# Performance work log

Measured on AMD Instinct MI355X. Metric: run time of the kernel, lower is better.

Reference implementation:

```python
import jax, jax.numpy as jnp
import numpy as np

N = 50000
E = 800000
H = 256
ED = 13
EPS = 1e-5


def silu(x):
    return x * jax.nn.sigmoid(x)


def layernorm(x, g, b):
    mu = jnp.mean(x, axis=-1, keepdims=True)
    var = jnp.var(x, axis=-1, keepdims=True)
    return (x - mu) * jax.lax.rsqrt(var + EPS) * g + b


def setup_inputs() -> dict:
    key = jax.random.key(0)
    ks = jax.random.split(key, 24)
    s = 0.02
    d = {
        "h": jax.random.normal(ks[0], (N, H), jnp.float32),
        "pos": jax.random.normal(ks[1], (N, 3), jnp.float32),
        "edge_index": jax.random.randint(ks[2], (2, E), 0, N, jnp.int32),
        "edge_attr": jax.random.normal(ks[3], (E, ED), jnp.float32),
        # edge_mlp: Linear(2H+1+ED -> 2H), SiLU, LN(2H), Linear(2H -> H), SiLU
        "W_e1": jax.random.normal(ks[4], (2 * H + 1 + ED, 2 * H), jnp.float32) * s,
        "b_e1": jnp.zeros((2 * H,), jnp.float32),
        "g_e": jnp.ones((2 * H,), jnp.float32),
        "be_ln": jnp.zeros((2 * H,), jnp.float32),
        "W_e2": jax.random.normal(ks[5], (2 * H, H), jnp.float32) * s,
        "b_e2": jnp.zeros((H,), jnp.float32),
        # node_mlp: Linear(2H -> 2H), SiLU, LN(2H), Linear(2H -> H)
        "W_n1": jax.random.normal(ks[6], (2 * H, 2 * H), jnp.float32) * s,
        "b_n1": jnp.zeros((2 * H,), jnp.float32),
        "g_n": jnp.ones((2 * H,), jnp.float32),
        "bn_ln": jnp.zeros((2 * H,), jnp.float32),
        "W_n2": jax.random.normal(ks[7], (2 * H, H), jnp.float32) * s,
        "b_n2": jnp.zeros((H,), jnp.float32),
        # outer LayerNorm(H)
        "g_o": jnp.ones((H,), jnp.float32),
        "bo_ln": jnp.zeros((H,), jnp.float32),
        # coord_mlp: Linear(H->H), SiLU, Linear(H->1, no bias, weight*0.001)
        "W_c1": jax.random.normal(ks[8], (H, H), jnp.float32) * s,
        "b_c1": jnp.zeros((H,), jnp.float32),
        "W_c2": jax.random.normal(ks[9], (H, 1), jnp.float32) * 0.001,
        # att_mlp: Linear(H->1), Sigmoid
        "W_a": jax.random.normal(ks[10], (H, 1), jnp.float32) * s,
        "b_a": jnp.zeros((1,), jnp.float32),
        # coord_feedback: Linear(1->H), SiLU, Linear(H->H)
        "W_f1": jax.random.normal(ks[11], (1, H), jnp.float32) * s,
        "b_f1": jnp.zeros((H,), jnp.float32),
        "W_f2": jax.random.normal(ks[12], (H, H), jnp.float32) * s,
        "b_f2": jnp.zeros((H,), jnp.float32),
    }
    return d


def reference(h, pos, edge_index, edge_attr,
              W_e1, b_e1, g_e, be_ln, W_e2, b_e2,
              W_n1, b_n1, g_n, bn_ln, W_n2, b_n2,
              g_o, bo_ln,
              W_c1, b_c1, W_c2,
              W_a, b_a,
              W_f1, b_f1, W_f2, b_f2):
    row, col = edge_index[0], edge_index[1]
    diff = pos[row] - pos[col]                                  # [E,3]
    dist = jnp.maximum(jnp.linalg.norm(diff, axis=-1, keepdims=True), 1e-5)
    edge_in = jnp.concatenate([h[row], h[col], dist, edge_attr], axis=-1)
    m = silu(layernorm(silu(edge_in @ W_e1 + b_e1), g_e, be_ln) @ W_e2 + b_e2)  # [E,H]
    att = jax.nn.sigmoid(m @ W_a + b_a)                         # [E,1]
    agg = jax.ops.segment_sum(m * att, row, num_segments=N)     # [N,H]
    node_in = jnp.concatenate([h, agg], axis=-1)
    h_upd = layernorm(silu(node_in @ W_n1 + b_n1), g_n, bn_ln) @ W_n2 + b_n2
    h_new = layernorm(h + h_upd, g_o, bo_ln)
    coord_w = silu(m @ W_c1 + b_c1) @ W_c2                      # [E,1]
    coord_agg = jax.ops.segment_sum(diff * coord_w, row, num_segments=N)
    pos_new = pos + coord_agg
    diff_new = pos_new[row] - pos_new[col]
    dist_new = jnp.maximum(jnp.linalg.norm(diff_new, axis=-1, keepdims=True), 1e-5)
    coord_fb = silu(dist_new @ W_f1 + b_f1) @ W_f2 + b_f2       # [E,H]
    fb_agg = jax.ops.segment_sum(coord_fb, row, num_segments=N)
    h_new = h_new + 0.1 * fb_agg
    return (h_new, pos_new)
```

## Files before the change

kernel.cpp:

```cpp
#include <hip/hip_runtime.h>


#define NN 50000
#define EE 800000

typedef unsigned short u16;
typedef float f32x4 __attribute__((ext_vector_type(4)));
typedef short bf16x8 __attribute__((ext_vector_type(8)));
typedef unsigned uint4v __attribute__((ext_vector_type(4)));

__device__ __forceinline__ u16 f2bf(float f) {
  unsigned u = __float_as_uint(f);
  u = (u + 0x7FFFu + ((u >> 16) & 1u)) >> 16;
  return (u16)u;
}
__device__ __forceinline__ float bf2f(u16 s) {
  return __uint_as_float(((unsigned)s) << 16);
}
__device__ __forceinline__ float bflo(unsigned u) { return __uint_as_float(u << 16); }
__device__ __forceinline__ float bfhi(unsigned u) { return __uint_as_float(u & 0xFFFF0000u); }
__device__ __forceinline__ float silu_f(float x) {
  return x * __builtin_amdgcn_rcpf(1.f + exp2f(x * -1.44269504f));
}

__device__ __forceinline__ void gload16(const void* g, void* l) {
  __builtin_amdgcn_global_load_lds(
      (const __attribute__((address_space(1))) void*)g,
      (__attribute__((address_space(3))) void*)l, 16, 0, 0);
}

__global__ __launch_bounds__(256, 2) void edge_fused(
    const u16* __restrict__ P1, const u16* __restrict__ P2,
    const float* __restrict__ dist, const float* __restrict__ eattr,
    const float* __restrict__ Wt, const float* __restrict__ ge,
    const float* __restrict__ beln, const float* __restrict__ be2,
    const float* __restrict__ bc1, const float* __restrict__ Wa,
    const float* __restrict__ ba, const float* __restrict__ Wc2,
    const u16* __restrict__ We2s, const u16* __restrict__ Wc1s,
    const int* __restrict__ rowp, const int* __restrict__ colp,
    const int* __restrict__ perm, const int* __restrict__ meta, int cidx,
    u16* __restrict__ mBuf, float* __restrict__ att, float* __restrict__ cwv) {
  const int M = meta[2 * cidx + 1];
  const int eb = meta[2 * cidx];
  const int m0 = blockIdx.x * 64;
  if (m0 >= M) return;
  __shared__ __align__(16) u16 At[64][512];
  __shared__ __align__(16) u16 Bs[4][64][32];
  const int tid = threadIdx.x, w = tid >> 6, lane = tid & 63;
  const int l15 = lane & 15, kq = lane >> 4;
  const int ch0 = lane * 8;
  const int sr = lane >> 2, sl = lane & 3;

  {
    float wreg[8][15], gg[8], bb[8];
#pragma unroll
    for (int i = 0; i < 8; i++) {
#pragma unroll
      for (int j = 0; j < 15; j++) wreg[i][j] = Wt[(ch0 + i) * 16 + j];
      gg[i] = ge[ch0 + i]; bb[i] = beln[ch0 + i];
    }
#pragma unroll 2
    for (int rr = 0; rr < 16; rr++) {
      int row = w * 16 + rr;
      int le = m0 + row; if (le > M - 1) le = M - 1;
      int e = perm[eb + le];
      int r = rowp[e], c = colp[e];
      float dd = dist[e];
      float fa[13];
#pragma unroll
      for (int j = 0; j < 13; j++) fa[j] = eattr[(size_t)e * 13 + j];
      uint4v u1 = *(const uint4v*)&P1[(size_t)r * 512 + ch0];
      uint4v u2 = *(const uint4v*)&P2[(size_t)c * 512 + ch0];
      float sv[8], s1 = 0.f, s2 = 0.f;
#pragma unroll
      for (int i = 0; i < 8; i++) {
        float xp = (i & 1) ? bfhi(u1[i >> 1]) : bflo(u1[i >> 1]);
        float xq = (i & 1) ? bfhi(u2[i >> 1]) : bflo(u2[i >> 1]);
        float x = xp + xq + wreg[i][0] + dd * wreg[i][1];
#pragma unroll
        for (int j = 0; j < 13; j++) x = fmaf(fa[j], wreg[i][2 + j], x);
        float s = silu_f(x);
        sv[i] = s; s1 += s; s2 += s * s;
      }
#pragma unroll
      for (int o = 32; o; o >>= 1) { s1 += __shfl_xor(s1, o); s2 += __shfl_xor(s2, o); }
      float mu = s1 * (1.f / 512.f);
      float inv = rsqrtf(s2 * (1.f / 512.f) - mu * mu + 1e-5f);
      u16 ot[8];
#pragma unroll
      for (int i = 0; i < 8; i++) ot[i] = f2bf((sv[i] - mu) * inv * gg[i] + bb[i]);
      *(uint4v*)&At[row][(lane ^ (row & 7)) * 8] = *(const uint4v*)ot;
    }
  }
  __syncthreads();

  f32x4 acc[4][4] = {};
  for (int k0 = 0; k0 < 512; k0 += 32) {
#pragma unroll
    for (int g = 0; g < 4; g++) {
      int r = w * 64 + g * 16 + sr;
      gload16(We2s + (size_t)r * 512 + k0 + sl * 8, &Bs[w][g * 16][0]);
    }
    __syncthreads();
    bf16x8 af[4], bfr[4];
#pragma unroll
    for (int i = 0; i < 4; i++) {
      int rw = i * 16 + l15;
      af[i] = *(const bf16x8*)&At[rw][(((k0 >> 3) + kq) ^ (rw & 7)) * 8];
    }
#pragma unroll
    for (int j = 0; j < 4; j++) {
      int rb = j * 16 + l15;
      bfr[j] = *(const bf16x8*)&Bs[w][rb][(kq ^ ((w * 64 + rb) & 3)) * 8];
    }
#pragma unroll
    for (int i = 0; i < 4; i++)
#pragma unroll
      for (int j = 0; j < 4; j++)
        acc[i][j] = __builtin_amdgcn_mfma_f32_16x16x32_bf16(af[i], bfr[j], acc[i][j], 0, 0, 0);
    __syncthreads();
  }

  u16* Mt = &At[0][0];
  float* red = (float*)&At[32][0];
  float ds_a[4][4];
#pragma unroll
  for (int i = 0; i < 4; i++)
#pragma unroll
    for (int t = 0; t < 4; t++) ds_a[i][t] = 0.f;
#pragma unroll
  for (int j = 0; j < 4; j++) {
    int col = w * 64 + j * 16 + l15;
    float bz = be2[col], wa = Wa[col];
    int slot = col >> 3, offc = col & 7;
#pragma unroll
    for (int i = 0; i < 4; i++) {
#pragma unroll
      for (int t = 0; t < 4; t++) {
        int row = i * 16 + kq * 4 + t;
        float sv = silu_f(acc[i][j][t] + bz);
        int le = m0 + row;
        if (le < M) mBuf[(size_t)le * 256 + col] = f2bf(sv);
        Mt[row * 256 + ((slot ^ (row & 7)) << 3) + offc] = f2bf(sv);
        ds_a[i][t] += sv * wa;
      }
    }
  }
#pragma unroll
  for (int i = 0; i < 4; i++)
#pragma unroll
    for (int t = 0; t < 4; t++) {
      float s = ds_a[i][t];
      s += __shfl_xor(s, 1); s += __shfl_xor(s, 2);
      s += __shfl_xor(s, 4); s += __shfl_xor(s, 8);
      if (l15 == 0) red[(i * 16 + kq * 4 + t) * 4 + w] = s;
    }
  __syncthreads();
  if (tid < 64) {
    int le = m0 + tid;
    if (le < M) {
      float s = red[tid * 4] + red[tid * 4 + 1] + red[tid * 4 + 2] + red[tid * 4 + 3] + ba[0];
      att[le] = __builtin_amdgcn_rcpf(1.f + exp2f(s * -1.44269504f));
    }
  }

  f32x4 ac2[4][4] = {};
  for (int k0 = 0; k0 < 256; k0 += 32) {
#pragma unroll
    for (int g = 0; g < 4; g++) {
      int r = w * 64 + g * 16 + sr;
      gload16(Wc1s + (size_t)r * 256 + k0 + sl * 8, &Bs[w][g * 16][0]);
    }
    __syncthreads();
    bf16x8 af[4], bfr[4];
#pragma unroll
    for (int i = 0; i < 4; i++) {
      int rw = i * 16 + l15;
      af[i] = *(const bf16x8*)&Mt[rw * 256 + ((((k0 >> 3) + kq) ^ (rw & 7)) << 3)];
    }
#pragma unroll
    for (int j = 0; j < 4; j++) {
      int rb = j * 16 + l15;
      bfr[j] = *(const bf16x8*)&Bs[w][rb][(kq ^ ((w * 64 + rb) & 3)) * 8];
    }
#pragma unroll
    for (int i = 0; i < 4; i++)
#pragma unroll
      for (int j = 0; j < 4; j++)
        ac2[i][j] = __builtin_amdgcn_mfma_f32_16x16x32_bf16(af[i], bfr[j], ac2[i][j], 0, 0, 0);
    __syncthreads();
  }
  float ds_c[4][4];
#pragma unroll
  for (int i = 0; i < 4; i++)
#pragma unroll
    for (int t = 0; t < 4; t++) ds_c[i][t] = 0.f;
#pragma unroll
  for (int j = 0; j < 4; j++) {
    int col = w * 64 + j * 16 + l15;
    float bz = bc1[col], wc = Wc2[col];
#pragma unroll
    for (int i = 0; i < 4; i++)
#pragma unroll
      for (int t = 0; t < 4; t++)
        ds_c[i][t] += silu_f(ac2[i][j][t] + bz) * wc;
  }
#pragma unroll
  for (int i = 0; i < 4; i++)
#pragma unroll
    for (int t = 0; t < 4; t++) {
      float s = ds_c[i][t];
      s += __shfl_xor(s, 1); s += __shfl_xor(s, 2);
      s += __shfl_xor(s, 4); s += __shfl_xor(s, 8);
      if (l15 == 0) red[(i * 16 + kq * 4 + t) * 4 + w] = s;
    }
  __syncthreads();
  if (tid < 64) {
    int le = m0 + tid;
    if (le < M)
      cwv[le] = red[tid * 4] + red[tid * 4 + 1] + red[tid * 4 + 2] + red[tid * 4 + 3];
  }
}

template <int MODE, int GATHER>
__global__ __launch_bounds__(256) void gemm128(
    const u16* __restrict__ A, const u16* __restrict__ BT,
    const float* __restrict__ bias, void* __restrict__ outp,
    int Mh, int Nc, int K,
    const u16* __restrict__ hbf, const u16* __restrict__ src2,
    const float* __restrict__ cnt, const float* __restrict__ b2, float scale) {
  const int M = Mh;
  const int m0 = blockIdx.x * 128, n0 = blockIdx.y * 128;
  if (m0 >= M) return;
  __shared__ __align__(16) u16 As[128][32];
  __shared__ __align__(16) u16 Bs[128][32];
  const int tid = threadIdx.x, w = tid >> 6, lane = tid & 63;
  const int srow = lane >> 2, sch = (lane & 3) * 8;
  const int r0 = w * 32 + srow, r1 = r0 + 16;

  u16* as0 = &As[w * 32][0];
  u16* as1 = &As[w * 32 + 16][0];
  u16* bs0 = &Bs[w * 32][0];
  u16* bs1 = &Bs[w * 32 + 16][0];

  const u16 *a0r, *a0c, *a1r, *a1c;
  a0c = a1c = nullptr;
  if (GATHER == 2) {
    int q0 = m0 + r0; if (q0 > M - 1) q0 = M - 1;
    int q1 = m0 + r1; if (q1 > M - 1) q1 = M - 1;
    a0r = hbf + (size_t)q0 * 256;  a0c = src2 + (size_t)q0 * 256;
    a1r = hbf + (size_t)q1 * 256;  a1c = src2 + (size_t)q1 * 256;
  } else {
    a0r = A + (size_t)(m0 + r0) * K;
    a1r = A + (size_t)(m0 + r1) * K;
  }
  const u16* b0 = BT + (size_t)(n0 + r0) * K;
  const u16* b1 = BT + (size_t)(n0 + r1) * K;

  f32x4 acc[4][4] = {};
  const int l15 = lane & 15, ko = (lane >> 4) * 8;
  const int ar0 = (w >> 1) * 64, br0 = (w & 1) * 64;

  for (int k0 = 0; k0 < K; k0 += 32) {
    const u16 *pa0, *pa1;
    if (GATHER == 2) {
      if (k0 < 256) { pa0 = a0r + k0;         pa1 = a1r + k0; }
      else          { pa0 = a0c + (k0 - 256); pa1 = a1c + (k0 - 256); }
    } else { pa0 = a0r + k0; pa1 = a1r + k0; }
    gload16(pa0 + sch, as0);
    gload16(pa1 + sch, as1);
    gload16(b0 + k0 + sch, bs0);
    gload16(b1 + k0 + sch, bs1);
    __syncthreads();
    bf16x8 af[4], bfr[4];
#pragma unroll
    for (int i = 0; i < 4; i++)
      af[i] = *reinterpret_cast<const bf16x8*>(&As[ar0 + i * 16 + l15][ko]);
#pragma unroll
    for (int j = 0; j < 4; j++)
      bfr[j] = *reinterpret_cast<const bf16x8*>(&Bs[br0 + j * 16 + l15][ko]);
#pragma unroll
    for (int i = 0; i < 4; i++)
#pragma unroll
      for (int j = 0; j < 4; j++)
        acc[i][j] = __builtin_amdgcn_mfma_f32_16x16x32_bf16(af[i], bfr[j], acc[i][j], 0, 0, 0);
    __syncthreads();
  }

  const int rb = m0 + ar0 + ((lane >> 4) << 2);
#pragma unroll
  for (int j = 0; j < 4; j++) {
    const int gc = n0 + br0 + j * 16 + l15;
    const float bz = (MODE == 2 || MODE == 7) ? 0.f : bias[gc];
#pragma unroll
    for (int i = 0; i < 4; i++) {
#pragma unroll
      for (int t = 0; t < 4; t++) {
        const int gr = rb + i * 16 + t;
        if (gr >= M) continue;
        float v = acc[i][j][t] + bz;
        size_t oi = (size_t)gr * Nc + gc;
        if (MODE == 0)      ((u16*)outp)[oi] = f2bf(silu_f(v));
        else if (MODE == 1) ((float*)outp)[oi] = v;
        else if (MODE == 2) ((float*)outp)[oi] += scale * (v + cnt[gr] * b2[gc]);
        else if (MODE == 7) ((u16*)outp)[oi] = f2bf(v);
      }
    }
  }
}

__global__ void wtrans(const float* __restrict__ src, u16* __restrict__ dst,
                       int K, int Nn, int Kpad) {
  int t = blockIdx.x * 256 + threadIdx.x;
  if (t >= Nn * Kpad) return;
  int n = t / Kpad, k = t - n * Kpad;
  float v = (k < K) ? src[(size_t)k * Nn + n] : 0.f;
  dst[t] = f2bf(v);
}

__global__ void wtrans_sw(const float* __restrict__ src, u16* __restrict__ dst,
                          int K, int Nn) {
  int t = blockIdx.x * 256 + threadIdx.x;
  if (t >= Nn * K) return;
  int n = t / K, kd = t - n * K;
  int ks = (kd & ~31) | (((((kd >> 3) & 3) ^ (n & 3))) << 3) | (kd & 7);
  dst[t] = f2bf(src[(size_t)ks * Nn + n]);
}

__global__ void build_wt(const float* __restrict__ W_e1, const float* __restrict__ b_e1,
                         float* __restrict__ Wt) {
  int t = blockIdx.x * 256 + threadIdx.x;
  if (t >= 512 * 16) return;
  int n = t >> 4, j = t & 15;
  float v = 0.f;
  if (j == 0) v = b_e1[n];
  else if (j < 15) v = W_e1[(size_t)(511 + j) * 512 + n];
  Wt[t] = v;
}

__global__ void edge_geom(const float* __restrict__ pos, const int* __restrict__ row,
                          const int* __restrict__ colx, float* __restrict__ dist,
                          int* __restrict__ icnt) {
  int e = blockIdx.x * 256 + threadIdx.x;
  if (e >= EE) return;
  int r = row[e], c = colx[e];
  float d0 = pos[r * 3 + 0] - pos[c * 3 + 0];
  float d1 = pos[r * 3 + 1] - pos[c * 3 + 1];
  float d2 = pos[r * 3 + 2] - pos[c * 3 + 2];
  dist[e] = fmaxf(sqrtf(d0 * d0 + d1 * d1 + d2 * d2), 1e-5f);
  atomicAdd(&icnt[r], 1);
}

__global__ __launch_bounds__(1024) void scan_ptr(const int* __restrict__ icnt,
                                                 int* __restrict__ ptr) {
  __shared__ int ls[1024];
  const int t = threadIdx.x;
  const int SEG = (NN + 1023) / 1024;
  int s0 = t * SEG;
  int s1 = s0 + SEG; if (s1 > NN) s1 = NN;
  int sum = 0;
  for (int i = s0; i < s1; i++) sum += icnt[i];
  ls[t] = sum;
  __syncthreads();
  for (int off = 1; off < 1024; off <<= 1) {
    int v = (t >= off) ? ls[t - off] : 0;
    __syncthreads();
    ls[t] += v;
    __syncthreads();
  }
  int run = ls[t] - sum;
  for (int i = s0; i < s1; i++) { ptr[i] = run; run += icnt[i]; }
  if (t == 1023) ptr[NN] = ls[1023];
}

__global__ void copy_head(const int* __restrict__ ptr, int* __restrict__ head,
                          float* __restrict__ cntf) {
  int n = blockIdx.x * 256 + threadIdx.x;
  if (n >= NN) return;
  head[n] = ptr[n];
  cntf[n] = (float)(ptr[n + 1] - ptr[n]);
}

__global__ void fill_perm(const int* __restrict__ row, int* __restrict__ head,
                          int* __restrict__ perm) {
  int e = blockIdx.x * 256 + threadIdx.x;
  if (e >= EE) return;
  int p = atomicAdd(&head[row[e]], 1);
  perm[p] = e;
}

__global__ void chunk_meta(const int* __restrict__ ptr, int* __restrict__ meta,
                           int CN, int nch, int capE) {
  int c = blockIdx.x * 256 + threadIdx.x;
  if (c >= nch) return;
  int lo = c * CN;
  int hi = lo + CN; if (hi > NN) hi = NN;
  int b = ptr[lo];
  int cc = ptr[hi] - b;
  if (cc > capE) cc = capE;
  meta[2 * c + 0] = b;
  meta[2 * c + 1] = cc;
}

__global__ __launch_bounds__(128) void ln_512(u16* __restrict__ t,
                                              const float* __restrict__ g,
                                              const float* __restrict__ b, int Mh) {
  int row = blockIdx.x;
  if (row >= Mh) return;
  int tid = threadIdx.x;
  size_t base = (size_t)row * 512 + tid * 4;
  ushort4 xv = *reinterpret_cast<const ushort4*>(&t[base]);
  float x0 = bf2f(xv.x), x1 = bf2f(xv.y), x2 = bf2f(xv.z), x3 = bf2f(xv.w);
  float s1 = x0 + x1 + x2 + x3;
  float s2 = x0 * x0 + x1 * x1 + x2 * x2 + x3 * x3;
  for (int o = 32; o; o >>= 1) { s1 += __shfl_xor(s1, o); s2 += __shfl_xor(s2, o); }
  __shared__ float red[4];
  if ((tid & 63) == 0) { red[tid >> 6] = s1; red[2 + (tid >> 6)] = s2; }
  __syncthreads();
  s1 = red[0] + red[1]; s2 = red[2] + red[3];
  float mu = s1 * (1.f / 512.f);
  float var = s2 * (1.f / 512.f) - mu * mu;
  float inv = rsqrtf(var + 1e-5f);
  int c = tid * 4;
  ushort4 yv;
  yv.x = f2bf((x0 - mu) * inv * g[c + 0] + b[c + 0]);
  yv.y = f2bf((x1 - mu) * inv * g[c + 1] + b[c + 1]);
  yv.z = f2bf((x2 - mu) * inv * g[c + 2] + b[c + 2]);
  yv.w = f2bf((x3 - mu) * inv * g[c + 3] + b[c + 3]);
  *reinterpret_cast<ushort4*>(&t[base]) = yv;
}

__global__ __launch_bounds__(256) void node_agg(
    const u16* __restrict__ m, const float* __restrict__ att,
    const float* __restrict__ cwv,
    const float* __restrict__ pos, const int* __restrict__ colx,
    const int* __restrict__ perm, const int* __restrict__ ptr,
    const int* __restrict__ meta, int cidx,
    u16* __restrict__ aggbf, float* __restrict__ cagg, int nlo, int cn) {
  int w = threadIdx.x >> 6, lane = threadIdx.x & 63;
  int nl = blockIdx.x * 4 + w;
  if (nl >= cn) return;
  int n = nlo + nl;
  int base = meta[2 * cidx];
  int p0 = ptr[n], p1 = ptr[n + 1];
  const int half = lane >> 5, ch = (lane & 31) * 8;
  float a[8] = {};
  for (int p = p0 + half; p < p1; p += 2) {
    int le = p - base;
    float at = att[le];
    uint4v mv = *reinterpret_cast<const uint4v*>(&m[(size_t)le * 256 + ch]);
#pragma unroll
    for (int i = 0; i < 4; i++) {
      a[2 * i]     += at * bflo(mv[i]);
      a[2 * i + 1] += at * bfhi(mv[i]);
    }
  }
#pragma unroll
  for (int i = 0; i < 8; i++) a[i] += __shfl_xor(a[i], 32);
  if (half == 0) {
    u16 ot[8];
#pragma unroll
    for (int i = 0; i < 8; i++) ot[i] = f2bf(a[i]);
    *reinterpret_cast<uint4v*>(&aggbf[(size_t)n * 256 + ch]) =
        *reinterpret_cast<const uint4v*>(ot);
  }
  float prx = pos[n * 3 + 0], pry = pos[n * 3 + 1], prz = pos[n * 3 + 2];
  float sx = 0.f, sy = 0.f, sz = 0.f;
  for (int p = p0 + lane; p < p1; p += 64) {
    int le = p - base;
    float cv = cwv[le];
    int c = colx[perm[p]];
    sx += cv * (prx - pos[c * 3 + 0]);
    sy += cv * (pry - pos[c * 3 + 1]);
    sz += cv * (prz - pos[c * 3 + 2]);
  }
#pragma unroll
  for (int o = 32; o; o >>= 1) {
    sx += __shfl_xor(sx, o); sy += __shfl_xor(sy, o); sz += __shfl_xor(sz, o);
  }
  if (lane == 0) {
    cagg[n * 3 + 0] = sx; cagg[n * 3 + 1] = sy; cagg[n * 3 + 2] = sz;
  }
}

__global__ __launch_bounds__(64) void hmid_ln(const float* __restrict__ h,
                                              const float* __restrict__ hupd,
                                              const float* __restrict__ g,
                                              const float* __restrict__ b,
                                              float* __restrict__ outp) {
  int row = blockIdx.x, lane = threadIdx.x;
  size_t base = (size_t)row * 256 + lane * 4;
  float x[4];
#pragma unroll
  for (int i = 0; i < 4; i++) x[i] = h[base + i] + hupd[base + i];
  float s1 = x[0] + x[1] + x[2] + x[3];
  float s2 = x[0] * x[0] + x[1] * x[1] + x[2] * x[2] + x[3] * x[3];
  for (int o = 32; o; o >>= 1) { s1 += __shfl_xor(s1, o); s2 += __shfl_xor(s2, o); }
  float mu = s1 * (1.f / 256.f);
  float var = s2 * (1.f / 256.f) - mu * mu;
  float inv = rsqrtf(var + 1e-5f);
#pragma unroll
  for (int i = 0; i < 4; i++)
    outp[base + i] = (x[i] - mu) * inv * g[lane * 4 + i] + b[lane * 4 + i];
}

__global__ void posnew_k(const float* __restrict__ pos, const float* __restrict__ cagg,
                         float* __restrict__ op) {
  int t = blockIdx.x * 256 + threadIdx.x;
  if (t >= NN * 3) return;
  op[t] = pos[t] + cagg[t];
}

__global__ void dnn_k(const float* __restrict__ posn, const int* __restrict__ rowp,
                      const int* __restrict__ colp, const int* __restrict__ perm,
                      float* __restrict__ dnc) {
  int p = blockIdx.x * 256 + threadIdx.x;
  if (p >= EE) return;
  int e = perm[p];
  int r = rowp[e], c = colp[e];
  float d0 = posn[r * 3 + 0] - posn[c * 3 + 0];
  float d1 = posn[r * 3 + 1] - posn[c * 3 + 1];
  float d2 = posn[r * 3 + 2] - posn[c * 3 + 2];
  dnc[p] = fmaxf(sqrtf(d0 * d0 + d1 * d1 + d2 * d2), 1e-5f);
}

__global__ __launch_bounds__(256) void edge_fb2(
    const float* __restrict__ dnc, const int* __restrict__ ptr,
    const float* __restrict__ Wf1, const float* __restrict__ bf1,
    u16* __restrict__ Sbf) {
  int w = threadIdx.x >> 6, lane = threadIdx.x & 63;
  int n = blockIdx.x * 4 + w;
  if (n >= NN) return;
  const float L2E = 1.44269504f;
  float w0 = Wf1[lane * 4 + 0], w1 = Wf1[lane * 4 + 1];
  float w2 = Wf1[lane * 4 + 2], w3 = Wf1[lane * 4 + 3];
  float b0 = bf1[lane * 4 + 0], b1 = bf1[lane * 4 + 1];
  float b2 = bf1[lane * 4 + 2], b3 = bf1[lane * 4 + 3];
  float wl0 = -w0 * L2E, wl1 = -w1 * L2E, wl2 = -w2 * L2E, wl3 = -w3 * L2E;
  float bl0 = -b0 * L2E, bl1 = -b1 * L2E, bl2 = -b2 * L2E, bl3 = -b3 * L2E;
  float a0 = 0.f, a1 = 0.f, a2 = 0.f, a3 = 0.f;
  int p0 = ptr[n], p1 = ptr[n + 1];
  for (int p = p0; p < p1; p++) {
    float dn = dnc[p];
    float x0 = fmaf(dn, w0, b0), e0 = exp2f(fmaf(dn, wl0, bl0));
    float x1 = fmaf(dn, w1, b1), e1 = exp2f(fmaf(dn, wl1, bl1));
    float x2 = fmaf(dn, w2, b2), e2 = exp2f(fmaf(dn, wl2, bl2));
    float x3 = fmaf(dn, w3, b3), e3 = exp2f(fmaf(dn, wl3, bl3));
    a0 += x0 * __builtin_amdgcn_rcpf(1.f + e0);
    a1 += x1 * __builtin_amdgcn_rcpf(1.f + e1);
    a2 += x2 * __builtin_amdgcn_rcpf(1.f + e2);
    a3 += x3 * __builtin_amdgcn_rcpf(1.f + e3);
  }
  ushort4 ov;
  ov.x = f2bf(a0); ov.y = f2bf(a1); ov.z = f2bf(a2); ov.w = f2bf(a3);
  *reinterpret_cast<ushort4*>(&Sbf[(size_t)n * 256 + lane * 4]) = ov;
}

__global__ void cvt_bf(const float* __restrict__ src, u16* __restrict__ dst, int n) {
  int t = blockIdx.x * 256 + threadIdx.x;
  if (t < n) dst[t] = f2bf(src[t]);
}

extern "C" void kernel_launch(void* const* d_in, const int* in_sizes, int n_in,
                              void* d_out, int out_size, void* d_ws, size_t ws_size,
                              hipStream_t stream) {
  const float* h     = (const float*)d_in[0];
  const float* pos   = (const float*)d_in[1];
  const int*   eidx  = (const int*)d_in[2];
  const float* eattr = (const float*)d_in[3];
  const float* W_e1 = (const float*)d_in[4];  const float* b_e1 = (const float*)d_in[5];
  const float* g_e  = (const float*)d_in[6];  const float* be_ln = (const float*)d_in[7];
  const float* W_e2 = (const float*)d_in[8];  const float* b_e2 = (const float*)d_in[9];
  const float* W_n1 = (const float*)d_in[10]; const float* b_n1 = (const float*)d_in[11];
  const float* g_n  = (const float*)d_in[12]; const float* bn_ln = (const float*)d_in[13];
  const float* W_n2 = (const float*)d_in[14]; const float* b_n2 = (const float*)d_in[15];
  const float* g_o  = (const float*)d_in[16]; const float* bo_ln = (const float*)d_in[17];
  const float* W_c1 = (const float*)d_in[18]; const float* b_c1 = (const float*)d_in[19];
  const float* W_c2 = (const float*)d_in[20];
  const float* W_a  = (const float*)d_in[21]; const float* b_a = (const float*)d_in[22];
  const float* W_f1 = (const float*)d_in[23]; const float* b_f1 = (const float*)d_in[24];
  const float* W_f2 = (const float*)d_in[25]; const float* b_f2 = (const float*)d_in[26];

  float* outp = (float*)d_out;
  float* out_pos = outp + (size_t)NN * 256;

  char* base = (char*)d_ws;
  size_t off = 0;
  auto alloc = [&](size_t bytes) -> void* {
    off = (off + 255) & ~(size_t)255;
    void* p = base + off;
    off += bytes;
    return p;
  };
  const int NP = 50048;
  u16* We1Ta = (u16*)alloc((size_t)512 * 256 * 2);
  u16* We1Tb = (u16*)alloc((size_t)512 * 256 * 2);
  u16* We2s  = (u16*)alloc((size_t)256 * 512 * 2);
  u16* Wc1s  = (u16*)alloc((size_t)256 * 256 * 2);
  u16* Wn1T  = (u16*)alloc((size_t)512 * 512 * 2);
  u16* Wn2T  = (u16*)alloc((size_t)256 * 512 * 2);
  u16* Wf2T  = (u16*)alloc((size_t)256 * 256 * 2);
  float* Wt  = (float*)alloc((size_t)512 * 16 * 4);
  u16* hbf   = (u16*)alloc((size_t)NP * 256 * 2);
  float* dist = (float*)alloc((size_t)EE * 4);
  int*   icnt = (int*)alloc((size_t)NN * 4);
  int*   ptr  = (int*)alloc((size_t)(NN + 1) * 4);
  int*   head = (int*)alloc((size_t)NN * 4);
  int*   perm = (int*)alloc((size_t)EE * 4);
  float* cntf = (float*)alloc((size_t)NN * 4);
  float* cagg = (float*)alloc((size_t)NN * 12);
  int*   meta = (int*)alloc((size_t)8192);
  u16*   aggbf = (u16*)alloc((size_t)NP * 256 * 2);
  u16*   P1 = (u16*)alloc((size_t)NP * 512 * 2);
  u16*   P2 = (u16*)alloc((size_t)NP * 512 * 2);

  off = (off + 255) & ~(size_t)255;
  char* arena = base + off;
  size_t avail = (ws_size > off) ? ws_size - off : 0;
  const size_t SBF_BYTES = (size_t)NP * 256 * 2;
  int CN = 8192;
  while (CN > 256) {
    size_t need = (size_t)(CN * 16 + 4096) * 520;
    if (need < SBF_BYTES) need = SBF_BYTES;
    if (need <= avail) break;
    CN >>= 1;
  }
  const int capE = CN * 16 + 4096;
  u16*   mBuf = (u16*)arena;
  float* att  = (float*)(arena + (size_t)capE * 512);
  float* cw   = (float*)(arena + (size_t)capE * 516);
  u16*   Sbf  = (u16*)arena;
  u16*   t2   = P1;
  float* hupd = (float*)P2;

  const int* rowp = eidx;
  const int* colp = eidx + EE;
  const int nch = (NN + CN - 1) / CN;

  hipMemsetAsync(icnt, 0, (size_t)NN * 4, stream);

  wtrans<<<(512 * 256 + 255) / 256, 256, 0, stream>>>(W_e1, We1Ta, 256, 512, 256);
  wtrans<<<(512 * 256 + 255) / 256, 256, 0, stream>>>(W_e1 + (size_t)256 * 512, We1Tb, 256, 512, 256);
  wtrans_sw<<<(256 * 512 + 255) / 256, 256, 0, stream>>>(W_e2, We2s, 512, 256);
  wtrans_sw<<<(256 * 256 + 255) / 256, 256, 0, stream>>>(W_c1, Wc1s, 256, 256);
  wtrans<<<(512 * 512 + 255) / 256, 256, 0, stream>>>(W_n1, Wn1T, 512, 512, 512);
  wtrans<<<(256 * 512 + 255) / 256, 256, 0, stream>>>(W_n2, Wn2T, 512, 256, 512);
  wtrans<<<(256 * 256 + 255) / 256, 256, 0, stream>>>(W_f2, Wf2T, 256, 256, 256);
  build_wt<<<(512 * 16 + 255) / 256, 256, 0, stream>>>(W_e1, b_e1, Wt);
  cvt_bf<<<(NN * 256 + 255) / 256, 256, 0, stream>>>(h, hbf, NN * 256);

  edge_geom<<<(EE + 255) / 256, 256, 0, stream>>>(pos, rowp, colp, dist, icnt);
  scan_ptr<<<1, 1024, 0, stream>>>(icnt, ptr);
  copy_head<<<(NN + 255) / 256, 256, 0, stream>>>(ptr, head, cntf);
  fill_perm<<<(EE + 255) / 256, 256, 0, stream>>>(rowp, head, perm);
  chunk_meta<<<(nch + 255) / 256, 256, 0, stream>>>(ptr, meta, CN, nch, capE);

  dim3 gp(NP / 128, 4);
  gemm128<7, 0><<<gp, 256, 0, stream>>>(hbf, We1Ta, nullptr, P1, NN, 512, 256,
                                        nullptr, nullptr, nullptr, nullptr, 0.f);
  gemm128<7, 0><<<gp, 256, 0, stream>>>(hbf, We1Tb, nullptr, P2, NN, 512, 256,
                                        nullptr, nullptr, nullptr, nullptr, 0.f);

  for (int c = 0; c < nch; c++) {
    int nlo = c * CN;
    int cn = NN - nlo; if (cn > CN) cn = CN;
    edge_fused<<<capE / 64, 256, 0, stream>>>(
        P1, P2, dist, eattr, Wt, g_e, be_ln, b_e2, b_c1, W_a, b_a, W_c2,
        We2s, Wc1s, rowp, colp, perm, meta, c, mBuf, att, cw);
    node_agg<<<(cn + 3) / 4, 256, 0, stream>>>(mBuf, att, cw, pos, colp, perm, ptr,
                                               meta, c, aggbf, cagg, nlo, cn);
  }

  gemm128<0, 2><<<gp, 256, 0, stream>>>(nullptr, Wn1T, b_n1, t2, NN, 512, 512,
                                        hbf, aggbf, nullptr, nullptr, 0.f);
  ln_512<<<NN, 128, 0, stream>>>(t2, g_n, bn_ln, NN);
  dim3 g5(NP / 128, 2);
  gemm128<1, 0><<<g5, 256, 0, stream>>>(t2, Wn2T, b_n2, hupd, NN, 256, 512,
                                        nullptr, nullptr, nullptr, nullptr, 0.f);
  hmid_ln<<<NN, 64, 0, stream>>>(h, hupd, g_o, bo_ln, outp);

  posnew_k<<<(NN * 3 + 255) / 256, 256, 0, stream>>>(pos, cagg, out_pos);
  dnn_k<<<(EE + 255) / 256, 256, 0, stream>>>(out_pos, rowp, colp, perm, dist);
  edge_fb2<<<(NN + 3) / 4, 256, 0, stream>>>(dist, ptr, W_f1, b_f1, Sbf);
  gemm128<2, 0><<<g5, 256, 0, stream>>>(Sbf, Wf2T, nullptr, outp, NN, 256, 256,
                                        nullptr, nullptr, cntf, b_f2, 0.1f);
}
```

Before: 2.191 ms.

## Load edge-MLP weights directly into MFMA fragment layout from global, drop LDS staging

```diff
diff --git a/kernel.cpp b/kernel.cpp
--- a/kernel.cpp
+++ b/kernel.cpp
@@ -36,7 +36,7 @@
     const float* __restrict__ beln, const float* __restrict__ be2,
     const float* __restrict__ bc1, const float* __restrict__ Wa,
     const float* __restrict__ ba, const float* __restrict__ Wc2,
-    const u16* __restrict__ We2s, const u16* __restrict__ Wc1s,
+    const u16* __restrict__ We2f, const u16* __restrict__ Wc1f,
     const int* __restrict__ rowp, const int* __restrict__ colp,
     const int* __restrict__ perm, const int* __restrict__ meta, int cidx,
     u16* __restrict__ mBuf, float* __restrict__ att, float* __restrict__ cwv) {
@@ -45,13 +45,18 @@
   const int m0 = blockIdx.x * 64;
   if (m0 >= M) return;
   __shared__ __align__(16) u16 At[64][512];
-  __shared__ __align__(16) u16 Bs[4][64][32];
   const int tid = threadIdx.x, w = tid >> 6, lane = tid & 63;
   const int l15 = lane & 15, kq = lane >> 4;
   const int ch0 = lane * 8;
-  const int sr = lane >> 2, sl = lane & 3;
 
   {
+    int le0 = m0 + w * 16 + (lane & 15);
+    if (le0 > M - 1) le0 = M - 1;
+    const int e_l = perm[eb + le0];
+    const int r_l = rowp[e_l];
+    const int c_l = colp[e_l];
+    const float dd_l = dist[e_l];
+
     float wreg[8][15], gg[8], bb[8];
 #pragma unroll
     for (int i = 0; i < 8; i++) {
@@ -61,11 +66,10 @@
     }
 #pragma unroll 2
     for (int rr = 0; rr < 16; rr++) {
-      int row = w * 16 + rr;
-      int le = m0 + row; if (le > M - 1) le = M - 1;
-      int e = perm[eb + le];
-      int r = rowp[e], c = colp[e];
-      float dd = dist[e];
+      int e = __shfl(e_l, rr);
+      int r = __shfl(r_l, rr);
+      int c = __shfl(c_l, rr);
+      float dd = __shfl(dd_l, rr);
       float fa[13];
 #pragma unroll
       for (int j = 0; j < 13; j++) fa[j] = eattr[(size_t)e * 13 + j];
@@ -86,6 +90,7 @@
       for (int o = 32; o; o >>= 1) { s1 += __shfl_xor(s1, o); s2 += __shfl_xor(s2, o); }
       float mu = s1 * (1.f / 512.f);
       float inv = rsqrtf(s2 * (1.f / 512.f) - mu * mu + 1e-5f);
+      int row = w * 16 + rr;
       u16 ot[8];
 #pragma unroll
       for (int i = 0; i < 8; i++) ot[i] = f2bf((sv[i] - mu) * inv * gg[i] + bb[i]);
@@ -95,31 +100,27 @@
   __syncthreads();
 
   f32x4 acc[4][4] = {};
-  for (int k0 = 0; k0 < 512; k0 += 32) {
-#pragma unroll
-    for (int g = 0; g < 4; g++) {
-      int r = w * 64 + g * 16 + sr;
-      gload16(We2s + (size_t)r * 512 + k0 + sl * 8, &Bs[w][g * 16][0]);
-    }
-    __syncthreads();
-    bf16x8 af[4], bfr[4];
-#pragma unroll
-    for (int i = 0; i < 4; i++) {
-      int rw = i * 16 + l15;
-      af[i] = *(const bf16x8*)&At[rw][(((k0 >> 3) + kq) ^ (rw & 7)) * 8];
-    }
-#pragma unroll
-    for (int j = 0; j < 4; j++) {
-      int rb = j * 16 + l15;
-      bfr[j] = *(const bf16x8*)&Bs[w][rb][(kq ^ ((w * 64 + rb) & 3)) * 8];
-    }
-#pragma unroll
-    for (int i = 0; i < 4; i++)
+  {
+    const u16* Bw = We2f + (size_t)w * 32768;
+#pragma unroll 4
+    for (int ks = 0; ks < 16; ks++) {
+      bf16x8 bfr[4], af[4];
 #pragma unroll
       for (int j = 0; j < 4; j++)
-        acc[i][j] = __builtin_amdgcn_mfma_f32_16x16x32_bf16(af[i], bfr[j], acc[i][j], 0, 0, 0);
-    __syncthreads();
-  }
+        bfr[j] = *(const bf16x8*)&Bw[((ks * 4 + j) * 64 + lane) * 8];
+#pragma unroll
+      for (int i = 0; i < 4; i++) {
+        int rw = i * 16 + l15;
+        af[i] = *(const bf16x8*)&At[rw][((ks * 4 + kq) ^ (rw & 7)) * 8];
+      }
+#pragma unroll
+      for (int i = 0; i < 4; i++)
+#pragma unroll
+        for (int j = 0; j < 4; j++)
+          acc[i][j] = __builtin_amdgcn_mfma_f32_16x16x32_bf16(af[i], bfr[j], acc[i][j], 0, 0, 0);
+    }
+  }
+  __syncthreads();
 
   u16* Mt = &At[0][0];
   float* red = (float*)&At[32][0];
@@ -165,30 +166,25 @@
   }
 
   f32x4 ac2[4][4] = {};
-  for (int k0 = 0; k0 < 256; k0 += 32) {
-#pragma unroll
-    for (int g = 0; g < 4; g++) {
-      int r = w * 64 + g * 16 + sr;
-      gload16(Wc1s + (size_t)r * 256 + k0 + sl * 8, &Bs[w][g * 16][0]);
-    }
-    __syncthreads();
-    bf16x8 af[4], bfr[4];
-#pragma unroll
-    for (int i = 0; i < 4; i++) {
-      int rw = i * 16 + l15;
-      af[i] = *(const bf16x8*)&Mt[rw * 256 + ((((k0 >> 3) + kq) ^ (rw & 7)) << 3)];
-    }
-#pragma unroll
-    for (int j = 0; j < 4; j++) {
-      int rb = j * 16 + l15;
-      bfr[j] = *(const bf16x8*)&Bs[w][rb][(kq ^ ((w * 64 + rb) & 3)) * 8];
-    }
-#pragma unroll
-    for (int i = 0; i < 4; i++)
+  {
+    const u16* Bw = Wc1f + (size_t)w * 16384;
+#pragma unroll 4
+    for (int ks = 0; ks < 8; ks++) {
+      bf16x8 bfr[4], af[4];
 #pragma unroll
       for (int j = 0; j < 4; j++)
-        ac2[i][j] = __builtin_amdgcn_mfma_f32_16x16x32_bf16(af[i], bfr[j], ac2[i][j], 0, 0, 0);
-    __syncthreads();
+        bfr[j] = *(const bf16x8*)&Bw[((ks * 4 + j) * 64 + lane) * 8];
+#pragma unroll
+      for (int i = 0; i < 4; i++) {
+        int rw = i * 16 + l15;
+        af[i] = *(const bf16x8*)&Mt[rw * 256 + (((ks * 4 + kq) ^ (rw & 7)) << 3)];
+      }
+#pragma unroll
+      for (int i = 0; i < 4; i++)
+#pragma unroll
+        for (int j = 0; j < 4; j++)
+          ac2[i][j] = __builtin_amdgcn_mfma_f32_16x16x32_bf16(af[i], bfr[j], ac2[i][j], 0, 0, 0);
+    }
   }
   float ds_c[4][4];
 #pragma unroll
@@ -318,13 +314,20 @@
   dst[t] = f2bf(v);
 }
 
-__global__ void wtrans_sw(const float* __restrict__ src, u16* __restrict__ dst,
-                          int K, int Nn) {
+__global__ void build_wf(const float* __restrict__ src, u16* __restrict__ dst,
+                         int K, int Nn) {
   int t = blockIdx.x * 256 + threadIdx.x;
   if (t >= Nn * K) return;
-  int n = t / K, kd = t - n * K;
-  int ks = (kd & ~31) | (((((kd >> 3) & 3) ^ (n & 3))) << 3) | (kd & 7);
-  dst[t] = f2bf(src[(size_t)ks * Nn + n]);
+  int i = t & 7;
+  int lane = (t >> 3) & 63;
+  int rest = t >> 9;
+  int j = rest & 3;
+  int rest2 = rest >> 2;
+  int KS = K >> 5;
+  int wv = rest2 / KS, ks = rest2 - wv * KS;
+  int n = wv * 64 + j * 16 + (lane & 15);
+  int k = ks * 32 + (lane >> 4) * 8 + i;
+  dst[t] = f2bf(src[(size_t)k * Nn + n]);
 }
 
 __global__ void build_wt(const float* __restrict__ W_e1, const float* __restrict__ b_e1,
@@ -595,8 +598,8 @@
   const int NP = 50048;
   u16* We1Ta = (u16*)alloc((size_t)512 * 256 * 2);
   u16* We1Tb = (u16*)alloc((size_t)512 * 256 * 2);
-  u16* We2s  = (u16*)alloc((size_t)256 * 512 * 2);
-  u16* Wc1s  = (u16*)alloc((size_t)256 * 256 * 2);
+  u16* We2f  = (u16*)alloc((size_t)256 * 512 * 2);
+  u16* Wc1f  = (u16*)alloc((size_t)256 * 256 * 2);
   u16* Wn1T  = (u16*)alloc((size_t)512 * 512 * 2);
   u16* Wn2T  = (u16*)alloc((size_t)256 * 512 * 2);
   u16* Wf2T  = (u16*)alloc((size_t)256 * 256 * 2);
@@ -641,8 +644,8 @@
 
   wtrans<<<(512 * 256 + 255) / 256, 256, 0, stream>>>(W_e1, We1Ta, 256, 512, 256);
   wtrans<<<(512 * 256 + 255) / 256, 256, 0, stream>>>(W_e1 + (size_t)256 * 512, We1Tb, 256, 512, 256);
-  wtrans_sw<<<(256 * 512 + 255) / 256, 256, 0, stream>>>(W_e2, We2s, 512, 256);
-  wtrans_sw<<<(256 * 256 + 255) / 256, 256, 0, stream>>>(W_c1, Wc1s, 256, 256);
+  build_wf<<<(256 * 512 + 255) / 256, 256, 0, stream>>>(W_e2, We2f, 512, 256);
+  build_wf<<<(256 * 256 + 255) / 256, 256, 0, stream>>>(W_c1, Wc1f, 256, 256);
   wtrans<<<(512 * 512 + 255) / 256, 256, 0, stream>>>(W_n1, Wn1T, 512, 512, 512);
   wtrans<<<(256 * 512 + 255) / 256, 256, 0, stream>>>(W_n2, Wn2T, 512, 256, 512);
   wtrans<<<(256 * 256 + 255) / 256, 256, 0, stream>>>(W_f2, Wf2T, 256, 256, 256);
@@ -666,7 +669,7 @@
     int cn = NN - nlo; if (cn > CN) cn = CN;
     edge_fused<<<capE / 64, 256, 0, stream>>>(
         P1, P2, dist, eattr, Wt, g_e, be_ln, b_e2, b_c1, W_a, b_a, W_c2,
-        We2s, Wc1s, rowp, colp, perm, meta, c, mBuf, att, cw);
+        We2f, Wc1f, rowp, colp, perm, meta, c, mBuf, att, cw);
     node_agg<<<(cn + 3) / 4, 256, 0, stream>>>(mBuf, att, cw, pos, colp, perm, ptr,
                                                meta, c, aggbf, cagg, nlo, cn);
   }
```

Measured after the change: 1.981 ms. 1.11x faster.
